# Kernel tuning notes

Measured on AMD Instinct MI355X. Metric: run time of the kernel, lower is better.

The kernel has to match this reference:

```python
import jax, jax.numpy as jnp
import numpy as np

DIM = 2048
N_EXPERTS = 16
TOP_K = 4
MOE_INTER = 1024
SHARED_INTER = 2 * MOE_INTER  # n_shared_experts * moe_inter_dim
B, S = 4, 1024
INIT = 0.02


def setup_inputs() -> dict:
    key = jax.random.key(0)
    ks = jax.random.split(key, 8)
    return {
        "x": jax.random.normal(ks[0], (B, S, DIM), dtype=jnp.float32),
        "gate_w": jax.random.normal(ks[1], (DIM, N_EXPERTS), dtype=jnp.float32) * INIT,
        "w1": jax.random.normal(ks[2], (N_EXPERTS, DIM, MOE_INTER), dtype=jnp.float32) * INIT,
        "w2": jax.random.normal(ks[3], (N_EXPERTS, MOE_INTER, DIM), dtype=jnp.float32) * INIT,
        "w3": jax.random.normal(ks[4], (N_EXPERTS, DIM, MOE_INTER), dtype=jnp.float32) * INIT,
        "ws1": jax.random.normal(ks[5], (DIM, SHARED_INTER), dtype=jnp.float32) * INIT,
        "ws2": jax.random.normal(ks[6], (SHARED_INTER, DIM), dtype=jnp.float32) * INIT,
        "ws3": jax.random.normal(ks[7], (DIM, SHARED_INTER), dtype=jnp.float32) * INIT,
    }


def _moe_forward(x, gate_w, w1, w2, w3, ws1, ws2, ws3):
    shape = x.shape
    xf = x.reshape(-1, DIM)  # [T, D]
    # Gate: softmax scores, top-k selection (weights are the top-k probs)
    scores = jax.nn.softmax(xf @ gate_w, axis=-1)          # [T, E]
    weights, indices = jax.lax.top_k(scores, TOP_K)         # [T, K] each
    y = jnp.zeros_like(xf)
    # Fixed loop over experts (structural, not over data dims).
    for e in range(N_EXPERTS):
        # gate coefficient for expert e: 0 if not in token's top-k
        coef = jnp.sum(weights * (indices == e), axis=-1)   # [T]
        h = jax.nn.silu(xf @ w1[e]) * (xf @ w3[e])          # [T, I]
        y = y + coef[:, None] * (h @ w2[e])
    # Shared experts (always-on gated MLP)
    z = (jax.nn.silu(xf @ ws1) * (xf @ ws3)) @ ws2
    return (y + z).reshape(shape)


def reference(x, gate_w, w1, w2, w3, ws1, ws2, ws3):
    return _moe_forward(x, gate_w, w1, w2, w3, ws1, ws2, ws3)
```

## Files before the change

kernel.cpp:

```cpp
#include <hip/hip_runtime.h>
#include <hip/hip_bf16.h>
#include <stdint.h>

#define T_TOK 4096
#define DIMD  2048
#define NEXP  16
#define TOPK  4
#define NI    1024
#define NSH   2048
#define TCAP  256

typedef __attribute__((ext_vector_type(8))) short short8;
typedef __attribute__((ext_vector_type(4))) float f32x4;
typedef __attribute__((ext_vector_type(4))) unsigned short u16x4;
typedef __attribute__((ext_vector_type(8))) unsigned short u16x8;

__device__ __forceinline__ unsigned short f2bf(float f) {
    union { float f; unsigned u; } v; v.f = f;
    return (unsigned short)((v.u + 0x7fffu + ((v.u >> 16) & 1u)) >> 16);
}

__device__ __forceinline__ float bf2f(unsigned short b) {
    union { unsigned u; float f; } v; v.u = (unsigned)b << 16;
    return v.f;
}

__device__ __forceinline__ void gload16(const void* g, void* l) {
    __builtin_amdgcn_global_load_lds(
        (const __attribute__((address_space(1))) void*)g,
        (__attribute__((address_space(3))) void*)l, 16, 0, 0);
}

__global__ __launch_bounds__(256) void gwt_kernel(const float* __restrict__ gw,
                                                  float* __restrict__ gwT) {
    int i = blockIdx.x * 256 + threadIdx.x;
    int d = i >> 4, e = i & 15;
    gwT[e * DIMD + d] = gw[i];
}

__global__ __launch_bounds__(256) void gate_kernel(const float* __restrict__ x,
                                                   const float* __restrict__ gwT,
                                                   int* __restrict__ blk_cnt,
                                                   int* __restrict__ tk_er,
                                                   float* __restrict__ tk_wv,
                                                   unsigned short* __restrict__ xb) {
    __shared__ int h[16];
    const int blk = blockIdx.x;
    const int t = blk * 4 + (threadIdx.x >> 6);
    const int lane = threadIdx.x & 63;
    if (threadIdx.x < 16) h[threadIdx.x] = 0;
    __syncthreads();

    const f32x4* xr = (const f32x4*)(x + (size_t)t * DIMD);
    f32x4 xv[8];
#pragma unroll
    for (int i = 0; i < 8; ++i) xv[i] = xr[i * 64 + lane];

    {
        unsigned short* xo = xb + (size_t)t * DIMD;
#pragma unroll
        for (int i = 0; i < 8; ++i) {
            u16x4 o;
#pragma unroll
            for (int j = 0; j < 4; ++j) o[j] = f2bf(xv[i][j]);
            *(u16x4*)(xo + i * 256 + lane * 4) = o;
        }
    }

    float acc[NEXP];
#pragma unroll
    for (int e = 0; e < NEXP; ++e) {
        const f32x4* gr = (const f32x4*)(gwT + e * DIMD);
        float s = 0.f;
#pragma unroll
        for (int i = 0; i < 8; ++i) {
            f32x4 gv = gr[i * 64 + lane];
            s += xv[i][0] * gv[0] + xv[i][1] * gv[1] +
                 xv[i][2] * gv[2] + xv[i][3] * gv[3];
        }
        acc[e] = s;
    }
#pragma unroll
    for (int e = 0; e < NEXP; ++e) {
        float v = acc[e];
#pragma unroll
        for (int off = 32; off; off >>= 1) v += __shfl_xor(v, off, 64);
        acc[e] = v;
    }
    float m = acc[0];
#pragma unroll
    for (int e = 1; e < NEXP; ++e) m = fmaxf(m, acc[e]);
    float s = 0.f;
#pragma unroll
    for (int e = 0; e < NEXP; ++e) { acc[e] = expf(acc[e] - m); s += acc[e]; }
    float inv = 1.f / s;
#pragma unroll
    for (int e = 0; e < NEXP; ++e) acc[e] *= inv;

    float w4[TOPK]; int i4[TOPK];
#pragma unroll
    for (int k = 0; k < TOPK; ++k) {
        float bv = -1.f; int be = 0;
#pragma unroll
        for (int e = 0; e < NEXP; ++e)
            if (acc[e] > bv) { bv = acc[e]; be = e; }
        w4[k] = bv; i4[k] = be;
#pragma unroll
        for (int e = 0; e < NEXP; ++e)
            if (e == be) acc[e] = -1.f;
    }

    if (lane == 0) {
        int r4[TOPK];
#pragma unroll
        for (int k = 0; k < TOPK; ++k) r4[k] = atomicAdd(&h[i4[k]], 1);
#pragma unroll
        for (int k = 0; k < TOPK; ++k) {
            tk_er[t * 4 + k] = (i4[k] << 20) | r4[k];
            tk_wv[t * 4 + k] = w4[k];
        }
    }
    __syncthreads();
    if (threadIdx.x < 16) blk_cnt[blk * 16 + threadIdx.x] = h[threadIdx.x];
}

__global__ __launch_bounds__(256) void scan_kernel(const int* __restrict__ blk_cnt,
                                                   int* __restrict__ blk_off,
                                                   int* __restrict__ cnt,
                                                   int* __restrict__ offs,
                                                   int* __restrict__ table) {
    __shared__ int gsum[16][17];
    __shared__ int gbase[16][17];
    __shared__ int csh[16];
    int tid = threadIdx.x;
    int e = tid >> 4, g = tid & 15;
    {
        int s = 0;
        for (int b = g * 64; b < g * 64 + 64; ++b) s += blk_cnt[b * 16 + e];
        gsum[e][g] = s;
    }
    __syncthreads();
    if (tid < 16) {
        int run = 0;
        for (int g2 = 0; g2 < 16; ++g2) { gbase[tid][g2] = run; run += gsum[tid][g2]; }
        csh[tid] = run;
        cnt[tid] = run;
    }
    __syncthreads();
    {
        int run = gbase[e][g];
        for (int b = g * 64; b < g * 64 + 64; ++b) {
            blk_off[b * 16 + e] = run;
            run += blk_cnt[b * 16 + e];
        }
    }
    if (tid == 0) {
        int o = 0;
        for (int e2 = 0; e2 < 16; ++e2) { offs[e2] = o; o += csh[e2]; }
        offs[NEXP] = o;
    }
    __syncthreads();
    for (int idx = tid; idx < 8 * TCAP; idx += 256) {
        int c = idx & 7, j = idx >> 3;
        int n0 = ((csh[c] + 255) >> 8) << 3;
        int n1 = ((csh[c + 8] + 255) >> 8) << 3;
        int v = -1;
        if (j < n0)
            v = (c << 16) | ((j & 7) << 13) | ((j >> 3) * 256);
        else if (j < n0 + n1) {
            int j2 = j - n0;
            v = ((c + 8) << 16) | ((j2 & 7) << 13) | ((j2 >> 3) * 256);
        }
        table[idx] = v;
    }
}

__global__ __launch_bounds__(256) void fill_kernel(const int* __restrict__ tk_er,
                                                   const float* __restrict__ tk_wv,
                                                   const int* __restrict__ blk_off,
                                                   const int* __restrict__ offs,
                                                   int* __restrict__ list,
                                                   float* __restrict__ cw,
                                                   int* __restrict__ rows) {
    int i = blockIdx.x * 256 + threadIdx.x;
    int rec = tk_er[i];
    int e = rec >> 20, r = rec & 0xFFFFF;
    int t = i >> 2;
    int ro = blk_off[(t >> 2) * 16 + e] + r;
    list[e * T_TOK + ro] = t;
    cw[e * T_TOK + ro] = tk_wv[i];
    rows[i] = offs[e] + ro;
}

__global__ __launch_bounds__(256) void tq_pair(const float* __restrict__ s1,
                                               const float* __restrict__ s3,
                                               unsigned short* __restrict__ dst,
                                               int K, int N,
                                               size_t srcStrideE, size_t dstStrideE) {
    int e = blockIdx.z;
    s1 += (size_t)e * srcStrideE;
    s3 += (size_t)e * srcStrideE;
    dst += (size_t)e * dstStrideE;
    __shared__ unsigned short tile[64][72];
    const int t = threadIdx.x;
    const int k0 = blockIdx.y * 64, n0 = blockIdx.x * 64;
    const int lr = t >> 4, lc4 = (t & 15) * 4;
    const int sr8 = (t & 7) * 8, sn = t >> 3;
#pragma unroll
    for (int half = 0; half < 2; ++half) {
        const float* src = half ? s3 : s1;
#pragma unroll
        for (int r = 0; r < 4; ++r) {
            f32x4 v = *(const f32x4*)(src + (size_t)(k0 + lr + r * 16) * N + n0 + lc4);
#pragma unroll
            for (int j = 0; j < 4; ++j) tile[lr + r * 16][lc4 + j] = f2bf(v[j]);
        }
        __syncthreads();
#pragma unroll
        for (int q = 0; q < 2; ++q) {
            int nn = sn + q * 32;
            int n = n0 + nn;
            int rrow = (n >> 4) * 32 + half * 16 + (n & 15);
            u16x8 o;
#pragma unroll
            for (int j = 0; j < 8; ++j) o[j] = tile[sr8 + j][nn];
            *(u16x8*)(dst + (size_t)rrow * K + k0 + sr8) = o;
        }
        __syncthreads();
    }
}

__global__ __launch_bounds__(256) void tq_plain(const float* __restrict__ src,
                                                unsigned short* __restrict__ dst,
                                                int K, int N,
                                                size_t srcStrideE, size_t dstStrideE) {
    int e = blockIdx.z;
    src += (size_t)e * srcStrideE;
    dst += (size_t)e * dstStrideE;
    __shared__ unsigned short tile[64][72];
    const int t = threadIdx.x;
    const int k0 = blockIdx.y * 64, n0 = blockIdx.x * 64;
    const int lr = t >> 4, lc4 = (t & 15) * 4;
    const int sr8 = (t & 7) * 8, sn = t >> 3;
#pragma unroll
    for (int r = 0; r < 4; ++r) {
        f32x4 v = *(const f32x4*)(src + (size_t)(k0 + lr + r * 16) * N + n0 + lc4);
#pragma unroll
        for (int j = 0; j < 4; ++j) tile[lr + r * 16][lc4 + j] = f2bf(v[j]);
    }
    __syncthreads();
#pragma unroll
    for (int q = 0; q < 2; ++q) {
        int nn = sn + q * 32;
        int n = n0 + nn;
        u16x8 o;
#pragma unroll
        for (int j = 0; j < 8; ++j) o[j] = tile[sr8 + j][nn];
        *(u16x8*)(dst + (size_t)n * K + k0 + sr8) = o;
    }
}

__global__ __launch_bounds__(256) void gather_kernel(const unsigned short* __restrict__ dbuf,
                                                     const int* __restrict__ rows,
                                                     float* __restrict__ out) {
    const int t = blockIdx.x;
    const int c8 = threadIdx.x * 8;
    int r[4];
#pragma unroll
    for (int k = 0; k < 4; ++k) r[k] = rows[t * 4 + k];
    f32x4 a0, a1;
    {
        const f32x4* z = (const f32x4*)(out + (size_t)t * DIMD + c8);
        a0 = z[0]; a1 = z[1];
    }
#pragma unroll
    for (int k = 0; k < 4; ++k) {
        u16x8 d = *(const u16x8*)(dbuf + (size_t)r[k] * DIMD + c8);
#pragma unroll
        for (int j = 0; j < 4; ++j) { a0[j] += bf2f(d[j]); a1[j] += bf2f(d[4 + j]); }
    }
    f32x4* o = (f32x4*)(out + (size_t)t * DIMD + c8);
    o[0] = a0; o[1] = a1;
}


#define BAR __builtin_amdgcn_s_barrier()
#define LGKM0 do { asm volatile("s_waitcnt lgkmcnt(0)" ::: "memory"); \
                   __builtin_amdgcn_sched_barrier(0); } while (0)

#define SA(H, D, KT) do { \
    gload16(pA[H][0] + (KT) * 64, (void*)(smem + (D) * 32768 + dofs[H][0])); \
    gload16(pA[H][1] + (KT) * 64, (void*)(smem + (D) * 32768 + dofs[H][1])); \
  } while (0)
#define SB(H, D, KT) do { \
    gload16(pB[H][0] + (KT) * 64, (void*)(smem + 65536 + (D) * 32768 + dofs[H][0])); \
    gload16(pB[H][1] + (KT) * 64, (void*)(smem + 65536 + (D) * 32768 + dofs[H][1])); \
  } while (0)

#define RDA(MH, D) do { \
    _Pragma("unroll") \
    for (int m2 = 0; m2 < 4; ++m2) { \
      const char* bp = smem + (D) * 32768 + wm * 16384 + ((MH) * 64 + m2 * 16 + fr) * 128; \
      aF[m2][0] = *(const short8*)(bp + kA0); \
      aF[m2][1] = *(const short8*)(bp + kA1); \
    } } while (0)
#define RDB(dst, NH, D) do { \
    _Pragma("unroll") \
    for (int n2 = 0; n2 < 2; ++n2) { \
      const char* bp = smem + 65536 + (D) * 32768 + (wn >> 1) * 16384 + \
                       ((wn & 1) * 64 + (NH) * 32 + n2 * 16 + fr) * 128; \
      dst[n2][0] = *(const short8*)(bp + kA0); \
      dst[n2][1] = *(const short8*)(bp + kA1); \
    } } while (0)

#define MM(MH, NH, BF) do { \
    __builtin_amdgcn_s_setprio(1); \
    _Pragma("unroll") \
    for (int m2 = 0; m2 < 4; ++m2) { \
      _Pragma("unroll") \
      for (int n2 = 0; n2 < 2; ++n2) { \
        acc[(MH) * 4 + m2][(NH) * 2 + n2] = __builtin_amdgcn_mfma_f32_16x16x32_bf16( \
            aF[m2][0], BF[n2][0], acc[(MH) * 4 + m2][(NH) * 2 + n2], 0, 0, 0); \
        acc[(MH) * 4 + m2][(NH) * 2 + n2] = __builtin_amdgcn_mfma_f32_16x16x32_bf16( \
            aF[m2][1], BF[n2][1], acc[(MH) * 4 + m2][(NH) * 2 + n2], 0, 0, 0); \
      } \
    } \
    __builtin_amdgcn_s_setprio(0); \
  } while (0)

template <bool UP>
__global__ __launch_bounds__(512, 2) void gemm_f(
    const unsigned short* __restrict__ Ash, const unsigned short* __restrict__ Art,
    const unsigned short* __restrict__ Bsh, const unsigned short* __restrict__ Brt,
    const int* __restrict__ cnt, const int* __restrict__ offs,
    const int* __restrict__ list, const float* __restrict__ cw,
    unsigned short* __restrict__ hs, unsigned short* __restrict__ hbuf,
    float* __restrict__ fout, unsigned short* __restrict__ dbuf,
    const int* __restrict__ table) {
    constexpr int SHBLK = UP ? 256 : 128;

    const int bid = blockIdx.x;
    const bool routed = bid >= SHBLK;
    int bx, rb, e = 0, M, obase = 0;
    const unsigned short* Ap;
    const unsigned short* Bp;
    int ASTRr, BSTRr;
    if (!routed) {
        if (UP) { bx = bid & 15; rb = (bid >> 4) * 256; }
        else    { bx = bid >> 4; rb = (bid & 15) * 256; }
        M = T_TOK;
        Ap = Ash; Bp = Bsh;
        ASTRr = 2048; BSTRr = 2048;
    } else {
        int pk = table[bid - SHBLK];
        if (pk < 0) return;
        e = pk >> 16; bx = (pk >> 13) & 7; rb = pk & 8191;
        M = cnt[e]; obase = offs[e];
        Ap = Art;
        Bp = Brt + (UP ? (size_t)e * 2048 * 2048 : (size_t)e * 2048 * 1024);
        ASTRr = UP ? 2048 : 1024;
        BSTRr = UP ? 2048 : 1024;
    }
    const int NT = UP ? 32 : (routed ? 16 : 32);

    extern __shared__ char smem[];

    const int tid = threadIdx.x;
    const int lane = tid & 63, wid = tid >> 6;
    const int wm = wid >> 2, wn = wid & 3;
    const int fr = lane & 15, fq = lane >> 4;
    const int s7 = fr & 7;
    const int kA0 = ((fq ^ s7) << 4);
    const int kA1 = kA0 ^ 64;

    const unsigned short* pA[2][2];
    const unsigned short* pB[2][2];
    int dofs[2][2];
#pragma unroll
    for (int h = 0; h < 2; ++h)
#pragma unroll
        for (int i = 0; i < 2; ++i) {
            int c = i * 512 + tid;
            int lr = c >> 3;
            int lsl = (c & 7) ^ (lr & 7);
            dofs[h][i] = h * 16384 + c * 16;
            int grA = rb + h * 128 + lr;
            int crA = (grA < M) ? grA : (M - 1);
            size_t arow;
            if (!routed)  arow = (size_t)grA;
            else if (UP)  arow = (size_t)list[e * T_TOK + crA];
            else          arow = (size_t)(obase + crA);
            pA[h][i] = Ap + arow * ASTRr + lsl * 8;
            pB[h][i] = Bp + (size_t)(bx * 256 + h * 128 + lr) * BSTRr + lsl * 8;
        }

    f32x4 acc[8][4];
#pragma unroll
    for (int m = 0; m < 8; ++m)
#pragma unroll
        for (int n = 0; n < 4; ++n) acc[m][n] = (f32x4)0.f;

    short8 aF[4][2], bF0[2][2], bF1[2][2];

    SB(0, 0, 0); SB(1, 0, 0); SA(0, 0, 0); SA(1, 0, 0);
    SB(0, 1, 1); SA(0, 1, 1);
    asm volatile("s_waitcnt vmcnt(4)" ::: "memory");
    BAR;

    for (int t = 0; t < NT; ++t) {
        const int D = t & 1;
        const bool m1 = (t + 1 < NT), m2g = (t + 2 < NT);
        RDA(0, D); RDB(bF0, 0, D);
        if (m1) SB(1, D ^ 1, t + 1);
        BAR; LGKM0;
        MM(0, 0, bF0);
        BAR;
        RDB(bF1, 1, D);
        if (m1) SA(1, D ^ 1, t + 1);
        BAR; LGKM0;
        MM(0, 1, bF1);
        BAR;
        RDA(1, D);
        if (m2g) SB(0, D, t + 2);
        BAR; LGKM0;
        MM(1, 1, bF1);
        BAR;
        if (m2g) SA(0, D, t + 2);
        MM(1, 0, bF0);
        if (m1) {
            if (m2g) { asm volatile("s_waitcnt vmcnt(4)" ::: "memory"); }
            else     { asm volatile("s_waitcnt vmcnt(0)" ::: "memory"); }
        }
        BAR;
    }

    if constexpr (UP) {
        const int LDO = routed ? NI : NSH;
        unsigned short* hp = routed ? hbuf : hs;
#pragma unroll
        for (int m = 0; m < 8; ++m)
#pragma unroll
            for (int q = 0; q < 4; ++q) {
                int gr = rb + wm * 128 + (m >> 2) * 64 + (m & 3) * 16 + fq * 4 + q;
                if (gr < M) {
                    float coef = routed ? cw[e * T_TOK + gr] : 1.f;
                    size_t orow = (size_t)((routed ? obase : 0) + gr) * LDO;
#pragma unroll
                    for (int j = 0; j < 2; ++j) {
                        float c1 = acc[m][2 * j][q], c3 = acc[m][2 * j + 1][q];
                        float hv = c1 / (1.f + __expf(-c1)) * c3 * coef;
                        int ncol = (bx * 8 + wn * 2 + j) * 16 + fr;
                        hp[orow + ncol] = f2bf(hv);
                    }
                }
            }
    } else {
#pragma unroll
        for (int m = 0; m < 8; ++m)
#pragma unroll
            for (int q = 0; q < 4; ++q) {
                int gr = rb + wm * 128 + (m >> 2) * 64 + (m & 3) * 16 + fq * 4 + q;
                if (gr < M) {
                    if (routed) {
                        unsigned short* op = dbuf + (size_t)(obase + gr) * DIMD;
#pragma unroll
                        for (int n = 0; n < 4; ++n) {
                            int col = bx * 256 + wn * 64 + (n >> 1) * 32 + (n & 1) * 16 + fr;
                            op[col] = f2bf(acc[m][n][q]);
                        }
                    } else {
                        float* op = fout + (size_t)gr * DIMD;
#pragma unroll
                        for (int n = 0; n < 4; ++n) {
                            int col = bx * 256 + wn * 64 + (n >> 1) * 32 + (n & 1) * 16 + fr;
                            op[col] = acc[m][n][q];
                        }
                    }
                }
            }
    }
}

extern "C" void kernel_launch(void* const* d_in, const int* in_sizes, int n_in,
                              void* d_out, int out_size, void* d_ws, size_t ws_size,
                              hipStream_t stream) {
    const float* x   = (const float*)d_in[0];
    const float* gw  = (const float*)d_in[1];
    const float* w1  = (const float*)d_in[2];
    const float* w2  = (const float*)d_in[3];
    const float* w3  = (const float*)d_in[4];
    const float* ws1 = (const float*)d_in[5];
    const float* ws2 = (const float*)d_in[6];
    const float* ws3 = (const float*)d_in[7];
    float* out = (float*)d_out;

    char* p = (char*)d_ws;
    unsigned short* xb   = (unsigned short*)p; p += (size_t)T_TOK * DIMD * 2;
    unsigned short* hs   = (unsigned short*)p; p += (size_t)T_TOK * NSH * 2;
    unsigned short* hbuf = (unsigned short*)p; p += (size_t)T_TOK * TOPK * NI * 2;
    unsigned short* upT  = (unsigned short*)p; p += (size_t)NEXP * 2048 * DIMD * 2;
    unsigned short* w2T  = (unsigned short*)p; p += (size_t)NEXP * DIMD * NI * 2;
    unsigned short* upsT = (unsigned short*)p; p += (size_t)2 * NSH * DIMD * 2;
    unsigned short* ws2T = (unsigned short*)p; p += (size_t)DIMD * NSH * 2;
    float* gwT = (float*)p;                    p += (size_t)NEXP * DIMD * 4;
    float* cw = (float*)p;                     p += (size_t)NEXP * T_TOK * 4;
    int* list = (int*)p;                       p += (size_t)NEXP * T_TOK * 4;
    int* tk_er = (int*)p;                      p += (size_t)T_TOK * TOPK * 4;
    float* tk_wv = (float*)p;                  p += (size_t)T_TOK * TOPK * 4;
    int* rows = (int*)p;                       p += (size_t)T_TOK * TOPK * 4;
    int* blk_cnt = (int*)p;                    p += (size_t)1024 * 16 * 4;
    int* blk_off = (int*)p;                    p += (size_t)1024 * 16 * 4;
    int* cnt = (int*)p;                        p += 256;
    int* offs = (int*)p;                       p += 256;
    int* table = (int*)p;                      p += 8192 * 4;
    if ((size_t)(p - (char*)d_ws) > ws_size) return;
    unsigned short* dbuf = upT;

    hipFuncSetAttribute((const void*)&gemm_f<true>, hipFuncAttributeMaxDynamicSharedMemorySize, 131072);
    hipFuncSetAttribute((const void*)&gemm_f<false>, hipFuncAttributeMaxDynamicSharedMemorySize, 131072);

    gwt_kernel<<<(NEXP * DIMD) / 256, 256, 0, stream>>>(gw, gwT);
    gate_kernel<<<T_TOK / 4, 256, 0, stream>>>(x, gwT, blk_cnt, tk_er, tk_wv, xb);
    scan_kernel<<<1, 256, 0, stream>>>(blk_cnt, blk_off, cnt, offs, table);
    fill_kernel<<<T_TOK * TOPK / 256, 256, 0, stream>>>(tk_er, tk_wv, blk_off, offs,
                                                        list, cw, rows);

    tq_pair<<<dim3(NI / 64, DIMD / 64, NEXP), 256, 0, stream>>>(
        w1, w3, upT, DIMD, NI, (size_t)DIMD * NI, (size_t)2048 * DIMD);
    tq_pair<<<dim3(NSH / 64, DIMD / 64, 1), 256, 0, stream>>>(
        ws1, ws3, upsT, DIMD, NSH, 0, 0);
    tq_plain<<<dim3(DIMD / 64, NI / 64, NEXP), 256, 0, stream>>>(
        w2, w2T, NI, DIMD, (size_t)NI * DIMD, (size_t)DIMD * NI);
    tq_plain<<<dim3(DIMD / 64, NSH / 64, 1), 256, 0, stream>>>(
        ws2, ws2T, NSH, DIMD, 0, 0);

    gemm_f<true><<<256 + 8 * TCAP, 512, 131072, stream>>>(
        xb, xb, upsT, upT, cnt, offs, list, cw, hs, hbuf, nullptr, nullptr, table);
    gemm_f<false><<<128 + 8 * TCAP, 512, 131072, stream>>>(
        hs, hbuf, ws2T, w2T, cnt, offs, list, nullptr, nullptr, nullptr, out, dbuf, table);
    gather_kernel<<<T_TOK, 256, 0, stream>>>(dbuf, rows, out);
}
```

Before: 585.9 us.

## Split up-projection into dedicated 128x256-tile kernel with 3-stage LDS pipeline

Replaces the templated up-projection GEMM with a separate kernel that uses 128-row tiles, a BK=32 triple-buffered LDS pipeline with 72KB shared memory, and a simpler single-buffer MFMA loop. A second dispatch table with 128-row granularity is built for the routed experts. The aim is better load balance and less padding waste for small per-expert token counts, and higher occupancy from the smaller LDS footprint. The cost is more blocks, less reuse per tile, and more barriers per unit of work.

```diff
diff --git a/kernel.cpp b/kernel.cpp
--- a/kernel.cpp
+++ b/kernel.cpp
@@ -8,7 +8,8 @@
 #define TOPK  4
 #define NI    1024
 #define NSH   2048
-#define TCAP  256
+#define TCAPU 320
+#define TCAPD 256
 
 typedef __attribute__((ext_vector_type(8))) short short8;
 typedef __attribute__((ext_vector_type(4))) float f32x4;
@@ -128,7 +129,8 @@
                                                    int* __restrict__ blk_off,
                                                    int* __restrict__ cnt,
                                                    int* __restrict__ offs,
-                                                   int* __restrict__ table) {
+                                                   int* __restrict__ table_u,
+                                                   int* __restrict__ table_d) {
     __shared__ int gsum[16][17];
     __shared__ int gbase[16][17];
     __shared__ int csh[16];
@@ -160,7 +162,20 @@
         offs[NEXP] = o;
     }
     __syncthreads();
-    for (int idx = tid; idx < 8 * TCAP; idx += 256) {
+    for (int idx = tid; idx < 8 * TCAPU; idx += 256) {
+        int c = idx & 7, j = idx >> 3;
+        int n0 = ((csh[c] + 127) >> 7) << 3;
+        int n1 = ((csh[c + 8] + 127) >> 7) << 3;
+        int v = -1;
+        if (j < n0)
+            v = (c << 16) | ((j & 7) << 13) | ((j >> 3) * 128);
+        else if (j < n0 + n1) {
+            int j2 = j - n0;
+            v = ((c + 8) << 16) | ((j2 & 7) << 13) | ((j2 >> 3) * 128);
+        }
+        table_u[idx] = v;
+    }
+    for (int idx = tid; idx < 8 * TCAPD; idx += 256) {
         int c = idx & 7, j = idx >> 3;
         int n0 = ((csh[c] + 255) >> 8) << 3;
         int n1 = ((csh[c + 8] + 255) >> 8) << 3;
@@ -171,7 +186,7 @@
             int j2 = j - n0;
             v = ((c + 8) << 16) | ((j2 & 7) << 13) | ((j2 >> 3) * 256);
         }
-        table[idx] = v;
+        table_d[idx] = v;
     }
 }
 
@@ -283,6 +298,129 @@
     o[0] = a0; o[1] = a1;
 }
 
+__global__ __launch_bounds__(512, 2) void gemm_up(
+    const unsigned short* __restrict__ xb, const unsigned short* __restrict__ upsT,
+    const unsigned short* __restrict__ upT,
+    const int* __restrict__ cnt, const int* __restrict__ offs,
+    const int* __restrict__ list, const float* __restrict__ cw,
+    unsigned short* __restrict__ hs, unsigned short* __restrict__ hbuf,
+    const int* __restrict__ table) {
+    constexpr int SHBLK = 512;
+    constexpr int NT = 64;
+
+    const int bid = blockIdx.x;
+    const bool routed = bid >= SHBLK;
+    int bx, rb, e = 0, M, obase = 0;
+    const unsigned short* Bp;
+    if (!routed) {
+        bx = bid & 15; rb = (bid >> 4) * 128;
+        M = T_TOK;
+        Bp = upsT;
+    } else {
+        int pk = table[bid - SHBLK];
+        if (pk < 0) return;
+        e = pk >> 16; bx = (pk >> 13) & 7; rb = pk & 8191;
+        M = cnt[e]; obase = offs[e];
+        Bp = upT + (size_t)e * 2048 * 2048;
+    }
+
+    extern __shared__ char smem[];
+
+    const int tid = threadIdx.x;
+    const int lane = tid & 63, wid = tid >> 6;
+    const int wm = wid >> 2, wn = wid & 3;
+    const int fr = lane & 15, fq = lane >> 4;
+    const int offR = ((fr >> 1) << 7) + (((((fr & 1) << 2) | fq) ^ (fr >> 1)) << 4);
+    const int d16 = tid * 16;
+
+    const unsigned short* pA;
+    const unsigned short* pB0;
+    const unsigned short* pB1;
+    {
+        int c = tid, s = c >> 3, sl = (c & 7) ^ (s & 7);
+        int rA = 2 * s + (sl >> 2), kk = (sl & 3) * 8;
+        int gr = rb + rA;
+        int cr = (gr < M) ? gr : (M - 1);
+        size_t arow = routed ? (size_t)list[e * T_TOK + cr] : (size_t)gr;
+        pA = xb + arow * 2048 + kk;
+    }
+#pragma unroll
+    for (int u = 0; u < 2; ++u) {
+        int c = u * 512 + tid, s = c >> 3, sl = (c & 7) ^ (s & 7);
+        int rB = 2 * s + (sl >> 2), kk = (sl & 3) * 8;
+        const unsigned short* p = Bp + (size_t)(bx * 256 + rB) * 2048 + kk;
+        if (u == 0) pB0 = p; else pB1 = p;
+    }
+
+    f32x4 acc[4][4];
+#pragma unroll
+    for (int m = 0; m < 4; ++m)
+#pragma unroll
+        for (int n = 0; n < 4; ++n) acc[m][n] = (f32x4)0.f;
+
+    gload16(pA,      (void*)(smem + 0 + d16));
+    gload16(pA + 32, (void*)(smem + 8192 + d16));
+    gload16(pB0,      (void*)(smem + 24576 + d16));
+    gload16(pB1,      (void*)(smem + 24576 + 8192 + d16));
+    gload16(pB0 + 32, (void*)(smem + 24576 + 16384 + d16));
+    gload16(pB1 + 32, (void*)(smem + 24576 + 16384 + 8192 + d16));
+    pA += 64; pB0 += 64; pB1 += 64;
+    asm volatile("s_waitcnt vmcnt(0)" ::: "memory");
+    __builtin_amdgcn_s_barrier();
+
+    int bA = 0, bA2 = 16384;
+    int bB = 0, bB2 = 32768;
+    for (int t = 0; t < NT; ++t) {
+        short8 aF[4], bF[4];
+#pragma unroll
+        for (int m = 0; m < 4; ++m)
+            aF[m] = *(const short8*)(smem + bA + wm * 4096 + m * 1024 + offR);
+#pragma unroll
+        for (int n = 0; n < 4; ++n)
+            bF[n] = *(const short8*)(smem + 24576 + bB + wn * 4096 + n * 1024 + offR);
+        const bool more = (t + 2 < NT);
+        if (more) {
+            gload16(pA, (void*)(smem + bA2 + d16));
+            gload16(pB0, (void*)(smem + 24576 + bB2 + d16));
+            gload16(pB1, (void*)(smem + 24576 + bB2 + 8192 + d16));
+            pA += 32; pB0 += 32; pB1 += 32;
+        }
+        __builtin_amdgcn_s_setprio(1);
+#pragma unroll
+        for (int m = 0; m < 4; ++m)
+#pragma unroll
+            for (int n = 0; n < 4; ++n)
+                acc[m][n] = __builtin_amdgcn_mfma_f32_16x16x32_bf16(aF[m], bF[n], acc[m][n], 0, 0, 0);
+        __builtin_amdgcn_s_setprio(0);
+        if (more) { asm volatile("s_waitcnt vmcnt(3)" ::: "memory"); }
+        else      { asm volatile("s_waitcnt vmcnt(0)" ::: "memory"); }
+        __builtin_amdgcn_s_barrier();
+        bA = (bA == 16384) ? 0 : bA + 8192;
+        bA2 = (bA2 == 16384) ? 0 : bA2 + 8192;
+        bB = (bB == 32768) ? 0 : bB + 16384;
+        bB2 = (bB2 == 32768) ? 0 : bB2 + 16384;
+    }
+
+    const int LDO = routed ? NI : NSH;
+    unsigned short* hp = routed ? hbuf : hs;
+#pragma unroll
+    for (int m = 0; m < 4; ++m)
+#pragma unroll
+        for (int q = 0; q < 4; ++q) {
+            int gr = rb + wm * 64 + m * 16 + fq * 4 + q;
+            if (gr < M) {
+                float coef = routed ? cw[e * T_TOK + gr] : 1.f;
+                size_t orow = (size_t)((routed ? obase : 0) + gr) * LDO;
+#pragma unroll
+                for (int nfp = 0; nfp < 2; ++nfp) {
+                    float c1 = acc[m][2 * nfp][q], c3 = acc[m][2 * nfp + 1][q];
+                    float h = c1 / (1.f + __expf(-c1)) * c3 * coef;
+                    int ncol = (bx * 8 + wn * 2 + nfp) * 16 + fr;
+                    hp[orow + ncol] = f2bf(h);
+                }
+            }
+        }
+}
 
 #define BAR __builtin_amdgcn_s_barrier()
 #define LGKM0 do { asm volatile("s_waitcnt lgkmcnt(0)" ::: "memory"); \
@@ -328,16 +466,14 @@
     __builtin_amdgcn_s_setprio(0); \
   } while (0)
 
-template <bool UP>
-__global__ __launch_bounds__(512, 2) void gemm_f(
-    const unsigned short* __restrict__ Ash, const unsigned short* __restrict__ Art,
-    const unsigned short* __restrict__ Bsh, const unsigned short* __restrict__ Brt,
+__global__ __launch_bounds__(512, 2) void gemm_dn(
+    const unsigned short* __restrict__ hsA, const unsigned short* __restrict__ hbufA,
+    const unsigned short* __restrict__ ws2T, const unsigned short* __restrict__ w2T,
     const int* __restrict__ cnt, const int* __restrict__ offs,
-    const int* __restrict__ list, const float* __restrict__ cw,
-    unsigned short* __restrict__ hs, unsigned short* __restrict__ hbuf,
+    const int* __restrict__ list,
     float* __restrict__ fout, unsigned short* __restrict__ dbuf,
     const int* __restrict__ table) {
-    constexpr int SHBLK = UP ? 256 : 128;
+    constexpr int SHBLK = 128;
 
     const int bid = blockIdx.x;
     const bool routed = bid >= SHBLK;
@@ -346,22 +482,20 @@
     const unsigned short* Bp;
     int ASTRr, BSTRr;
     if (!routed) {
-        if (UP) { bx = bid & 15; rb = (bid >> 4) * 256; }
-        else    { bx = bid >> 4; rb = (bid & 15) * 256; }
+        bx = bid >> 4; rb = (bid & 15) * 256;
         M = T_TOK;
-        Ap = Ash; Bp = Bsh;
+        Ap = hsA; Bp = ws2T;
         ASTRr = 2048; BSTRr = 2048;
     } else {
         int pk = table[bid - SHBLK];
         if (pk < 0) return;
         e = pk >> 16; bx = (pk >> 13) & 7; rb = pk & 8191;
         M = cnt[e]; obase = offs[e];
-        Ap = Art;
-        Bp = Brt + (UP ? (size_t)e * 2048 * 2048 : (size_t)e * 2048 * 1024);
-        ASTRr = UP ? 2048 : 1024;
-        BSTRr = UP ? 2048 : 1024;
-    }
-    const int NT = UP ? 32 : (routed ? 16 : 32);
+        Ap = hbufA;
+        Bp = w2T + (size_t)e * 2048 * 1024;
+        ASTRr = 1024; BSTRr = 1024;
+    }
+    const int NT = routed ? 16 : 32;
 
     extern __shared__ char smem[];
 
@@ -386,10 +520,7 @@
             dofs[h][i] = h * 16384 + c * 16;
             int grA = rb + h * 128 + lr;
             int crA = (grA < M) ? grA : (M - 1);
-            size_t arow;
-            if (!routed)  arow = (size_t)grA;
-            else if (UP)  arow = (size_t)list[e * T_TOK + crA];
-            else          arow = (size_t)(obase + crA);
+            size_t arow = routed ? (size_t)(obase + crA) : (size_t)grA;
             pA[h][i] = Ap + arow * ASTRr + lsl * 8;
             pB[h][i] = Bp + (size_t)(bx * 256 + h * 128 + lr) * BSTRr + lsl * 8;
         }
@@ -434,51 +565,29 @@
         BAR;
     }
 
-    if constexpr (UP) {
-        const int LDO = routed ? NI : NSH;
-        unsigned short* hp = routed ? hbuf : hs;
-#pragma unroll
-        for (int m = 0; m < 8; ++m)
-#pragma unroll
-            for (int q = 0; q < 4; ++q) {
-                int gr = rb + wm * 128 + (m >> 2) * 64 + (m & 3) * 16 + fq * 4 + q;
-                if (gr < M) {
-                    float coef = routed ? cw[e * T_TOK + gr] : 1.f;
-                    size_t orow = (size_t)((routed ? obase : 0) + gr) * LDO;
-#pragma unroll
-                    for (int j = 0; j < 2; ++j) {
-                        float c1 = acc[m][2 * j][q], c3 = acc[m][2 * j + 1][q];
-                        float hv = c1 / (1.f + __expf(-c1)) * c3 * coef;
-                        int ncol = (bx * 8 + wn * 2 + j) * 16 + fr;
-                        hp[orow + ncol] = f2bf(hv);
+#pragma unroll
+    for (int m = 0; m < 8; ++m)
+#pragma unroll
+        for (int q = 0; q < 4; ++q) {
+            int gr = rb + wm * 128 + (m >> 2) * 64 + (m & 3) * 16 + fq * 4 + q;
+            if (gr < M) {
+                if (routed) {
+                    unsigned short* op = dbuf + (size_t)(obase + gr) * DIMD;
+#pragma unroll
+                    for (int n = 0; n < 4; ++n) {
+                        int col = bx * 256 + wn * 64 + (n >> 1) * 32 + (n & 1) * 16 + fr;
+                        op[col] = f2bf(acc[m][n][q]);
+                    }
+                } else {
+                    float* op = fout + (size_t)gr * DIMD;
+#pragma unroll
+                    for (int n = 0; n < 4; ++n) {
+                        int col = bx * 256 + wn * 64 + (n >> 1) * 32 + (n & 1) * 16 + fr;
+                        op[col] = acc[m][n][q];
                     }
                 }
             }
-    } else {
-#pragma unroll
-        for (int m = 0; m < 8; ++m)
-#pragma unroll
-            for (int q = 0; q < 4; ++q) {
-                int gr = rb + wm * 128 + (m >> 2) * 64 + (m & 3) * 16 + fq * 4 + q;
-                if (gr < M) {
-                    if (routed) {
-                        unsigned short* op = dbuf + (size_t)(obase + gr) * DIMD;
-#pragma unroll
-                        for (int n = 0; n < 4; ++n) {
-                            int col = bx * 256 + wn * 64 + (n >> 1) * 32 + (n & 1) * 16 + fr;
-                            op[col] = f2bf(acc[m][n][q]);
-                        }
-                    } else {
-                        float* op = fout + (size_t)gr * DIMD;
-#pragma unroll
-                        for (int n = 0; n < 4; ++n) {
-                            int col = bx * 256 + wn * 64 + (n >> 1) * 32 + (n & 1) * 16 + fr;
-                            op[col] = acc[m][n][q];
-                        }
-                    }
-                }
-            }
-    }
+        }
 }
 
 extern "C" void kernel_launch(void* const* d_in, const int* in_sizes, int n_in,
@@ -512,16 +621,17 @@
     int* blk_off = (int*)p;                    p += (size_t)1024 * 16 * 4;
     int* cnt = (int*)p;                        p += 256;
     int* offs = (int*)p;                       p += 256;
-    int* table = (int*)p;                      p += 8192 * 4;
+    int* table_u = (int*)p;                    p += 8 * TCAPU * 4;
+    int* table_d = (int*)p;                    p += 8 * TCAPD * 4;
     if ((size_t)(p - (char*)d_ws) > ws_size) return;
     unsigned short* dbuf = upT;
 
-    hipFuncSetAttribute((const void*)&gemm_f<true>, hipFuncAttributeMaxDynamicSharedMemorySize, 131072);
-    hipFuncSetAttribute((const void*)&gemm_f<false>, hipFuncAttributeMaxDynamicSharedMemorySize, 131072);
+    hipFuncSetAttribute((const void*)&gemm_up, hipFuncAttributeMaxDynamicSharedMemorySize, 73728);
+    hipFuncSetAttribute((const void*)&gemm_dn, hipFuncAttributeMaxDynamicSharedMemorySize, 131072);
 
     gwt_kernel<<<(NEXP * DIMD) / 256, 256, 0, stream>>>(gw, gwT);
     gate_kernel<<<T_TOK / 4, 256, 0, stream>>>(x, gwT, blk_cnt, tk_er, tk_wv, xb);
-    scan_kernel<<<1, 256, 0, stream>>>(blk_cnt, blk_off, cnt, offs, table);
+    scan_kernel<<<1, 256, 0, stream>>>(blk_cnt, blk_off, cnt, offs, table_u, table_d);
     fill_kernel<<<T_TOK * TOPK / 256, 256, 0, stream>>>(tk_er, tk_wv, blk_off, offs,
                                                         list, cw, rows);
 
@@ -534,9 +644,9 @@
     tq_plain<<<dim3(DIMD / 64, NSH / 64, 1), 256, 0, stream>>>(
         ws2, ws2T, NSH, DIMD, 0, 0);
 
-    gemm_f<true><<<256 + 8 * TCAP, 512, 131072, stream>>>(
-        xb, xb, upsT, upT, cnt, offs, list, cw, hs, hbuf, nullptr, nullptr, table);
-    gemm_f<false><<<128 + 8 * TCAP, 512, 131072, stream>>>(
-        hs, hbuf, ws2T, w2T, cnt, offs, list, nullptr, nullptr, nullptr, out, dbuf, table);
+    gemm_up<<<512 + 8 * TCAPU, 512, 73728, stream>>>(
+        xb, upsT, upT, cnt, offs, list, cw, hs, hbuf, table_u);
+    gemm_dn<<<128 + 8 * TCAPD, 512, 131072, stream>>>(
+        hs, hbuf, ws2T, w2T, cnt, offs, list, out, dbuf, table_d);
     gather_kernel<<<T_TOK, 256, 0, stream>>>(dbuf, rows, out);
 }
```

Measured after the change: 584.7 us. Within noise of the previous version (-0.2%).
